# Kernel tuning notes

Measured on AMD Instinct MI355X. Metric: run time of the kernel, lower is better.

## Reference

```python
import jax, jax.numpy as jnp
import numpy as np

B, S, D = 4, 2048, 768
H = 12
DH = D // H
FF = 4 * D
EPS = 1e-5


def _layernorm(x, g, b):
    mu = jnp.mean(x, axis=-1, keepdims=True)
    var = jnp.mean(jnp.square(x - mu), axis=-1, keepdims=True)
    return (x - mu) * jax.lax.rsqrt(var + EPS) * g + b


def setup_inputs() -> dict:
    key = jax.random.key(0)
    ks = jax.random.split(key, 16)
    s_d = 1.0 / np.sqrt(D)
    s_ff = 1.0 / np.sqrt(FF)
    inp = {
        "x": jax.random.normal(ks[0], (B, S, D), jnp.float32),
        # LayerNorm 1
        "ln1_g": jnp.ones((D,), jnp.float32),
        "ln1_b": jnp.zeros((D,), jnp.float32),
        # attention linears (stored as [in, out], i.e. already transposed)
        "Wq": jax.random.normal(ks[1], (D, D), jnp.float32) * s_d,
        "bq": jax.random.normal(ks[2], (D,), jnp.float32) * s_d,
        "Wk": jax.random.normal(ks[3], (D, D), jnp.float32) * s_d,
        "bk": jax.random.normal(ks[4], (D,), jnp.float32) * s_d,
        "Wv": jax.random.normal(ks[5], (D, D), jnp.float32) * s_d,
        "bv": jax.random.normal(ks[6], (D,), jnp.float32) * s_d,
        "Wo": jax.random.normal(ks[7], (D, D), jnp.float32) * s_d,
        "bo": jax.random.normal(ks[8], (D,), jnp.float32) * s_d,
        # LayerNorm 2
        "ln2_g": jnp.ones((D,), jnp.float32),
        "ln2_b": jnp.zeros((D,), jnp.float32),
        # feed-forward (bias always on, per torch code)
        "W1": jax.random.normal(ks[9], (D, FF), jnp.float32) * s_d,
        "b1": jax.random.normal(ks[10], (FF,), jnp.float32) * s_d,
        "W2": jax.random.normal(ks[11], (FF, D), jnp.float32) * s_ff,
        "b2": jax.random.normal(ks[12], (D,), jnp.float32) * s_ff,
    }
    return inp


def reference(x, ln1_g, ln1_b, Wq, bq, Wk, bk, Wv, bv, Wo, bo,
              ln2_g, ln2_b, W1, b1, W2, b2):
    # --- attention branch (pre-LN) ---
    h = _layernorm(x, ln1_g, ln1_b)
    q = (h @ Wq + bq).reshape(B, S, H, DH).transpose(0, 2, 1, 3)  # [B,H,S,DH]
    k = (h @ Wk + bk).reshape(B, S, H, DH).transpose(0, 2, 1, 3)
    v = (h @ Wv + bv).reshape(B, S, H, DH).transpose(0, 2, 1, 3)
    scores = jnp.einsum("bhqd,bhkd->bhqk", q, k) / np.sqrt(DH)
    causal = jnp.tril(jnp.ones((S, S), bool))
    scores = jnp.where(causal, scores, -jnp.inf)
    attn = jax.nn.softmax(scores, axis=-1)
    out = jnp.einsum("bhqk,bhkd->bhqd", attn, v)
    out = out.transpose(0, 2, 1, 3).reshape(B, S, D)
    x = x + (out @ Wo + bo)
    # --- feed-forward branch (pre-LN, exact GELU) ---
    h2 = _layernorm(x, ln2_g, ln2_b)
    ff = jax.nn.gelu(h2 @ W1 + b1, approximate=False) @ W2 + b2
    return x + ff
```

## Files before the change

### kernel.cpp

```cpp
#include <hip/hip_runtime.h>
#include <math.h>

#define B_ 4
#define S_ 2048
#define D_ 768
#define H_ 12
#define DH_ 64
#define FF_ 3072
#define LDQ (3*D_)

using short8  = __attribute__((ext_vector_type(8))) short;
using f32x4   = __attribute__((ext_vector_type(4))) float;
using f32x16  = __attribute__((ext_vector_type(16))) float;
using float4v = __attribute__((ext_vector_type(4))) float;
using ushort4v= __attribute__((ext_vector_type(4))) unsigned short;

__device__ __forceinline__ unsigned short f2bf(float f) {
  unsigned u = __builtin_bit_cast(unsigned, f);
  u += 0x7FFFu + ((u >> 16) & 1u);
  return (unsigned short)(u >> 16);
}

__device__ __forceinline__ unsigned cvt_pk_bf16(float a, float b) {
  unsigned r;
  asm("v_cvt_pk_bf16_f32 %0, %1, %2" : "=v"(r) : "v"(a), "v"(b));
  return r;
}

__device__ __forceinline__ void gload16(const void* g, void* l) {
  __builtin_amdgcn_global_load_lds(
      (const __attribute__((address_space(1))) unsigned*)g,
      (__attribute__((address_space(3))) unsigned*)l, 16, 0, 0);
}

__global__ __launch_bounds__(256) void transpose_cast_multi_kernel(
    const float* __restrict__ Wq, const float* __restrict__ Wk,
    const float* __restrict__ Wv, const float* __restrict__ Wo,
    const float* __restrict__ W1, const float* __restrict__ W2,
    unsigned short* __restrict__ WqT, unsigned short* __restrict__ WkT,
    unsigned short* __restrict__ WvT, unsigned short* __restrict__ WoT,
    unsigned short* __restrict__ W1T, unsigned short* __restrict__ W2T) {
  __shared__ float tile[32][33];
  int bid = blockIdx.x;
  const float* in; unsigned short* out; int K, N, t;
  if (bid < 2304) {
    int seg = bid / 576; t = bid % 576; K = D_; N = D_;
    in  = seg == 0 ? Wq  : seg == 1 ? Wk  : seg == 2 ? Wv  : Wo;
    out = seg == 0 ? WqT : seg == 1 ? WkT : seg == 2 ? WvT : WoT;
  } else if (bid < 4608) {
    t = bid - 2304; K = D_; N = FF_; in = W1; out = W1T;
  } else {
    t = bid - 4608; K = FF_; N = D_; in = W2; out = W2T;
  }
  int ntk = K / 32;
  int k0 = (t % ntk) * 32, n0 = (t / ntk) * 32;
  int tx = threadIdx.x, ty = threadIdx.y;
#pragma unroll
  for (int i = 0; i < 4; i++)
    tile[ty + 8*i][tx] = in[(size_t)(k0 + ty + 8*i) * N + n0 + tx];
  __syncthreads();
#pragma unroll
  for (int i = 0; i < 4; i++)
    out[(size_t)(n0 + ty + 8*i) * K + k0 + tx] = f2bf(tile[tx][ty + 8*i]);
}

__global__ void bias_cat_kernel(const float* __restrict__ bq, const float* __restrict__ bk,
                                const float* __restrict__ bv, float* __restrict__ dst) {
  int i = blockIdx.x * 256 + threadIdx.x;
  if (i >= 3 * D_) return;
  float v;
  if (i < D_)            v = bq[i];
  else if (i < 2 * D_)   v = bk[i - D_];
  else                   v = bv[i - 2 * D_];
  dst[i] = v;
}

__global__ __launch_bounds__(256) void layernorm_kernel(
    const float* __restrict__ x, const float* __restrict__ g,
    const float* __restrict__ b, unsigned short* __restrict__ out) {
  int wave = threadIdx.x >> 6, lane = threadIdx.x & 63;
  int row = blockIdx.x * 4 + wave;
  const float* xr = x + (size_t)row * D_;
  float4v v[3];
  float sum = 0.f, sq = 0.f;
#pragma unroll
  for (int i = 0; i < 3; i++) {
    v[i] = reinterpret_cast<const float4v*>(xr)[lane + 64*i];
#pragma unroll
    for (int j = 0; j < 4; j++) { sum += v[i][j]; sq += v[i][j]*v[i][j]; }
  }
#pragma unroll
  for (int d = 1; d < 64; d <<= 1) { sum += __shfl_xor(sum, d); sq += __shfl_xor(sq, d); }
  float mu   = sum * (1.0f / D_);
  float var  = sq  * (1.0f / D_) - mu * mu;
  float rstd = rsqrtf(var + 1e-5f);
  unsigned short* orow = out + (size_t)row * D_;
#pragma unroll
  for (int i = 0; i < 3; i++) {
    int idx = (lane + 64*i) * 4;
    ushort4v o;
#pragma unroll
    for (int j = 0; j < 4; j++)
      o[j] = f2bf((v[i][j] - mu) * rstd * g[idx + j] + b[idx + j]);
    *reinterpret_cast<ushort4v*>(orow + idx) = o;
  }
}

#define EPI_QKV   0
#define EPI_OPROJ 1
#define EPI_GELU  2
#define EPI_FINAL 3

template<int EPI>
__global__ __launch_bounds__(256) void gemm_kernel(
    const unsigned short* __restrict__ A, int lda,
    const unsigned short* __restrict__ BT, int K,
    const float* __restrict__ bias,
    const float* __restrict__ resid,
    float* __restrict__ outf,
    unsigned short* __restrict__ outh,
    int ldo, float ascale, int nN) {
  __shared__ __attribute__((aligned(16))) unsigned short Ls[3][128*64];
  int tid = threadIdx.x;
  int wave = tid >> 6, lane = tid & 63;
  int lrow = lane & 15, lk = lane >> 4;
  int bid = blockIdx.x;
  int xcd = bid & 7, j = bid >> 3;
  int nM8 = gridDim.x / (8 * nN);
  int m0 = (xcd * nM8 + j / nN) * 128;
  int n0 = (j % nN) * 128;
  int wm = (wave >> 1) * 64, wn = (wave & 1) * 64;

  auto STAGE = [&](int buf, int k0) {
#pragma unroll
    for (int i = 0; i < 4; i++) {
      int ch = i * 256 + tid;
      int row = ch >> 3, s8 = ch & 7;
      int m = s8 ^ (row & 7);
      const unsigned short* src = (m < 4)
        ? A  + (size_t)(m0 + row) * lda + k0 + m * 8
        : BT + (size_t)(n0 + row) * K   + k0 + (m - 4) * 8;
      gload16(src, &Ls[buf][(i*256 + wave*64) * 8]);
    }
  };

  f32x4 acc[4][4] = {};
  int nt = K / 32;
  STAGE(0, 0);
  STAGE(1, 32);
  for (int t = 0; t < nt; t++) {
    if (t + 1 < nt) { asm volatile("s_waitcnt vmcnt(4)" ::: "memory"); }
    else            { asm volatile("s_waitcnt vmcnt(0)" ::: "memory"); }
    __builtin_amdgcn_s_barrier();
    const unsigned short* Lc = Ls[t % 3];
    short8 af[4], bf[4];
#pragma unroll
    for (int mi = 0; mi < 4; mi++) {
      int row = wm + mi*16 + lrow;
      af[mi] = *reinterpret_cast<const short8*>(&Lc[row*64 + ((lk ^ (row & 7)) * 8)]);
    }
#pragma unroll
    for (int ni = 0; ni < 4; ni++) {
      int row = wn + ni*16 + lrow;
      bf[ni] = *reinterpret_cast<const short8*>(&Lc[row*64 + (((4 + lk) ^ (row & 7)) * 8)]);
    }
    if (t + 2 < nt) STAGE((t + 2) % 3, (t + 2) * 32);
    __builtin_amdgcn_s_setprio(1);
#pragma unroll
    for (int mi = 0; mi < 4; mi++)
#pragma unroll
      for (int ni = 0; ni < 4; ni++)
        acc[mi][ni] = __builtin_amdgcn_mfma_f32_16x16x32_bf16(af[mi], bf[ni], acc[mi][ni], 0, 0, 0);
    __builtin_amdgcn_s_setprio(0);
  }
#pragma unroll
  for (int mi = 0; mi < 4; mi++) {
#pragma unroll
    for (int ni = 0; ni < 4; ni++) {
#pragma unroll
      for (int r = 0; r < 4; r++) {
        int gm = m0 + wm + mi*16 + (lane >> 4)*4 + r;
        int gn = n0 + wn + ni*16 + lrow;
        float v = acc[mi][ni][r] + bias[gn];
        if constexpr (EPI == EPI_QKV) {
          if (gn < D_) v *= ascale;
          outh[(size_t)gm * ldo + gn] = f2bf(v);
        } else if constexpr (EPI == EPI_OPROJ) {
          size_t idx = (size_t)gm * ldo + gn;
          outf[idx] = v + resid[idx];
        } else if constexpr (EPI == EPI_GELU) {
          float gv = 0.5f * v * (1.0f + erff(v * 0.70710678118654752f));
          outh[(size_t)gm * ldo + gn] = f2bf(gv);
        } else {
          size_t idx = (size_t)gm * ldo + gn;
          outf[idx] = v + resid[idx];
        }
      }
    }
  }
}

__global__ __launch_bounds__(256) void attn_kernel(
    const unsigned short* __restrict__ qkv,
    unsigned short* __restrict__ o) {
  __shared__ __attribute__((aligned(16))) unsigned short Ks[2][64*64];
  __shared__ __attribute__((aligned(16))) unsigned short VT[2][64*64];
  __shared__ __attribute__((aligned(16))) unsigned short P2[4][32*64];
  int tid = threadIdx.x;
  int wave = tid >> 6, lane = tid & 63;
  int ql = lane & 31, hi = lane >> 5;
  int bid = blockIdx.x;
  int xcd = bid & 7, r = bid >> 3;
  int bh = xcd * 6 + (r % 6);
  int qtile = 15 - (r / 6);
  int bb = bh / H_, hh = bh % H_;
  const unsigned short* qb = qkv + (size_t)bb * S_ * LDQ + hh * DH_;
  const unsigned short* kb = qb + D_;
  const unsigned short* vb = qb + 2 * D_;
  unsigned short* Pw = P2[wave];
  int swq = (ql & 7) << 4;

  int sr = tid >> 2;
  int sc16 = (tid & 3) * 16;
  int kp = tid & 31, dh0 = (tid >> 5) * 8;
  uint4 krA, krB, vrA, vrB;

  auto LOADR = [&](int kb0) {
    const unsigned short* ksrc = kb + (size_t)(kb0 + sr) * LDQ + sc16;
    krA = *reinterpret_cast<const uint4*>(ksrc);
    krB = *reinterpret_cast<const uint4*>(ksrc + 8);
    const unsigned short* vsrc = vb + (size_t)(kb0 + 2*kp) * LDQ + dh0;
    vrA = *reinterpret_cast<const uint4*>(vsrc);
    vrB = *reinterpret_cast<const uint4*>(vsrc + LDQ);
  };
  auto WRITE = [&](int buf) {
    int sw = (sr & 7) << 4;
    int cb = sc16 * 2;
    *reinterpret_cast<uint4*>(&Ks[buf][(sr*128 + (cb ^ sw)) >> 1]) = krA;
    *reinterpret_cast<uint4*>(&Ks[buf][(sr*128 + ((cb + 16) ^ sw)) >> 1]) = krB;
    union { uint4 u4; unsigned short s[8]; } a, b;
    a.u4 = vrA; b.u4 = vrB;
#pragma unroll
    for (int j2 = 0; j2 < 8; j2++) {
      int row = dh0 + j2, sw2 = (row & 7) << 4;
      *reinterpret_cast<unsigned*>(&VT[buf][(row*128 + ((4*kp) ^ sw2)) >> 1]) =
          (unsigned)a.s[j2] | ((unsigned)b.s[j2] << 16);
    }
  };

  int q0 = qtile * 128;
  int qw = q0 + wave * 32;
  int myq = qw + ql;

  short8 qf[4];
#pragma unroll
  for (int dblk = 0; dblk < 4; dblk++)
    qf[dblk] = *reinterpret_cast<const short8*>(qb + (size_t)myq * LDQ + dblk*16 + hi*8);

  f32x16 oaccT[2] = {};
  float mst = -1e30f, lst = 0.f;
  int nt = q0 / 64 + 2;

  LOADR(0);
  WRITE(0);
  __syncthreads();

  for (int kt = 0; kt < nt; kt++) {
    int kb0 = kt * 64;
    int cur = kt & 1;
    if (kt + 1 < nt) LOADR((kt + 1) * 64);

    if (kb0 <= qw + 31) {
      f32x16 sc[2] = {};
      __builtin_amdgcn_s_setprio(1);
#pragma unroll
      for (int dblk = 0; dblk < 4; dblk++) {
#pragma unroll
        for (int blk = 0; blk < 2; blk++) {
          int row = blk*32 + ql;
          int sw = (row & 7) << 4;
          short8 kf = *reinterpret_cast<const short8*>(
              &Ks[cur][(row*128 + (((unsigned)(dblk*32 + hi*16)) ^ sw)) >> 1]);
          sc[blk] = __builtin_amdgcn_mfma_f32_32x32x16_bf16(kf, qf[dblk], sc[blk], 0, 0, 0);
        }
      }
      __builtin_amdgcn_s_setprio(0);
      bool full = (kb0 + 63 <= qw);
      if (!full) {
#pragma unroll
        for (int blk = 0; blk < 2; blk++)
#pragma unroll
          for (int r2 = 0; r2 < 16; r2++) {
            int key = kb0 + blk*32 + (r2 & 3) + 8*(r2 >> 2) + 4*hi;
            if (key > myq) sc[blk][r2] = -1e30f;
          }
      }
      float pm0 = -1e30f, pm1 = -1e30f, pm2 = -1e30f, pm3 = -1e30f;
#pragma unroll
      for (int blk = 0; blk < 2; blk++)
#pragma unroll
        for (int g = 0; g < 4; g++) {
          pm0 = fmaxf(pm0, sc[blk][4*g]);
          pm1 = fmaxf(pm1, sc[blk][4*g+1]);
          pm2 = fmaxf(pm2, sc[blk][4*g+2]);
          pm3 = fmaxf(pm3, sc[blk][4*g+3]);
        }
      float mx = fmaxf(fmaxf(pm0, pm1), fmaxf(pm2, pm3));
      mx = fmaxf(mx, __shfl_xor(mx, 32));
      if (!__all(mx <= mst + 8.0f)) {
        float mnew = fmaxf(mst, mx);
        float fac = exp2f(mst - mnew);
        lst *= fac;
#pragma unroll
        for (int db = 0; db < 2; db++)
#pragma unroll
          for (int r2 = 0; r2 < 16; r2++) oaccT[db][r2] *= fac;
        mst = mnew;
      }
      float ps0 = 0.f, ps1 = 0.f, ps2 = 0.f, ps3 = 0.f;
#pragma unroll
      for (int blk = 0; blk < 2; blk++)
#pragma unroll
        for (int g = 0; g < 4; g++) {
          float p0 = exp2f(sc[blk][4*g]   - mst);
          float p1 = exp2f(sc[blk][4*g+1] - mst);
          float p2 = exp2f(sc[blk][4*g+2] - mst);
          float p3 = exp2f(sc[blk][4*g+3] - mst);
          ps0 += p0; ps1 += p1; ps2 += p2; ps3 += p3;
          uint2 val;
          val.x = cvt_pk_bf16(p0, p1);
          val.y = cvt_pk_bf16(p2, p3);
          int cbyte = (blk*64 + g*16 + hi*8) ^ swq;
          *reinterpret_cast<uint2*>(&Pw[(ql*128 + cbyte) >> 1]) = val;
        }
      float rs = (ps0 + ps1) + (ps2 + ps3);
      rs += __shfl_xor(rs, 32);
      lst += rs;
      __builtin_amdgcn_s_setprio(1);
#pragma unroll
      for (int ks = 0; ks < 4; ks++) {
        int cb = ks*32 + hi*16;
        short8 pa = *reinterpret_cast<const short8*>(&Pw[(ql*128 + (cb ^ swq)) >> 1]);
#pragma unroll
        for (int db = 0; db < 2; db++) {
          int row = db*32 + ql;
          int sw = (row & 7) << 4;
          short8 vf = *reinterpret_cast<const short8*>(&VT[cur][(row*128 + (cb ^ sw)) >> 1]);
          oaccT[db] = __builtin_amdgcn_mfma_f32_32x32x16_bf16(vf, pa, oaccT[db], 0, 0, 0);
        }
      }
      __builtin_amdgcn_s_setprio(0);
    }

    if (kt + 1 < nt) WRITE((kt + 1) & 1);
    __syncthreads();
  }

  float inv = 1.0f / lst;
  unsigned short* ob = o + ((size_t)(bb * S_ + myq)) * D_ + hh * DH_;
#pragma unroll
  for (int db = 0; db < 2; db++)
#pragma unroll
    for (int g = 0; g < 8; g++) {
      int r2 = 2 * g;
      int dh = db*32 + (r2 & 3) + 8*(r2 >> 2) + 4*hi;
      unsigned pk = cvt_pk_bf16(oaccT[db][r2] * inv, oaccT[db][r2+1] * inv);
      *reinterpret_cast<unsigned*>(ob + dh) = pk;
    }
}

extern "C" void kernel_launch(void* const* d_in, const int* in_sizes, int n_in,
                              void* d_out, int out_size, void* d_ws, size_t ws_size,
                              hipStream_t stream) {
  (void)in_sizes; (void)n_in; (void)out_size; (void)ws_size;
  const float* x    = (const float*)d_in[0];
  const float* ln1g = (const float*)d_in[1];
  const float* ln1b = (const float*)d_in[2];
  const float* Wq   = (const float*)d_in[3];
  const float* bq   = (const float*)d_in[4];
  const float* Wk   = (const float*)d_in[5];
  const float* bk   = (const float*)d_in[6];
  const float* Wv   = (const float*)d_in[7];
  const float* bv   = (const float*)d_in[8];
  const float* Wo   = (const float*)d_in[9];
  const float* bo   = (const float*)d_in[10];
  const float* ln2g = (const float*)d_in[11];
  const float* ln2b = (const float*)d_in[12];
  const float* W1   = (const float*)d_in[13];
  const float* b1   = (const float*)d_in[14];
  const float* W2   = (const float*)d_in[15];
  const float* b2   = (const float*)d_in[16];
  float* out = (float*)d_out;

  char* ws = (char*)d_ws;
  size_t off = 0;
  auto alloc = [&](size_t bytes) {
    char* p = ws + off;
    off += (bytes + 255) & ~(size_t)255;
    return p;
  };
  unsigned short* WqT = (unsigned short*)alloc((size_t)D_*D_*2);
  unsigned short* WkT = (unsigned short*)alloc((size_t)D_*D_*2);
  unsigned short* WvT = (unsigned short*)alloc((size_t)D_*D_*2);
  unsigned short* WoT = (unsigned short*)alloc((size_t)D_*D_*2);
  unsigned short* W1T = (unsigned short*)alloc((size_t)D_*FF_*2);
  unsigned short* W2T = (unsigned short*)alloc((size_t)FF_*D_*2);
  unsigned short* h   = (unsigned short*)alloc((size_t)B_*S_*D_*2);
  unsigned short* qkv = (unsigned short*)alloc((size_t)B_*S_*LDQ*2);
  unsigned short* ob  = (unsigned short*)alloc((size_t)B_*S_*D_*2);
  float* bias_cat     = (float*)alloc((size_t)3*D_*4);
  unsigned short* ffb = qkv;
  unsigned short* h2  = h;

  const float qscale = 0.125f * 1.4426950408889634f;

  dim3 tb(32, 8);
  transpose_cast_multi_kernel<<<6912, tb, 0, stream>>>(
      Wq, Wk, Wv, Wo, W1, W2, WqT, WkT, WvT, WoT, W1T, W2T);
  bias_cat_kernel<<<9, 256, 0, stream>>>(bq, bk, bv, bias_cat);

  layernorm_kernel<<<(B_*S_)/4, 256, 0, stream>>>(x, ln1g, ln1b, h);

  gemm_kernel<EPI_QKV><<<dim3(64*18), 256, 0, stream>>>(
      h, D_, WqT, D_, bias_cat, nullptr, nullptr, qkv, LDQ, qscale, 18);

  attn_kernel<<<dim3(768), 256, 0, stream>>>(qkv, ob);

  gemm_kernel<EPI_OPROJ><<<dim3(64*6), 256, 0, stream>>>(
      ob, D_, WoT, D_, bo, x, out, nullptr, D_, 1.0f, 6);

  layernorm_kernel<<<(B_*S_)/4, 256, 0, stream>>>(out, ln2g, ln2b, h2);

  gemm_kernel<EPI_GELU><<<dim3(64*24), 256, 0, stream>>>(
      h2, D_, W1T, D_, b1, nullptr, nullptr, ffb, FF_, 1.0f, 24);

  gemm_kernel<EPI_FINAL><<<dim3(64*6), 256, 0, stream>>>(
      ffb, FF_, W2T, FF_, b2, out, out, nullptr, D_, 1.0f, 6);
}
```

Before: 278.3 us.

## Split causal attention across key ranges with a pairing and a merge kernel

The attention kernel now pairs query tile p with tile 15-p. Each block processes the first part of one tile's key range and the second part of the other's, so every block runs the same number of key tiles instead of between 2 and 32. Each pass writes unnormalized bf16 partial outputs plus its running max and sum to a workspace buffer. A new merge kernel rescales and combines the two partials per query row and writes the normalized output. This trades the causal load imbalance for an extra kernel launch, extra global traffic for the partials, and a small bf16 rounding step on the intermediate results.

```diff
diff --git a/kernel.cpp b/kernel.cpp
--- a/kernel.cpp
+++ b/kernel.cpp
@@ -19,6 +19,11 @@
   unsigned u = __builtin_bit_cast(unsigned, f);
   u += 0x7FFFu + ((u >> 16) & 1u);
   return (unsigned short)(u >> 16);
+}
+
+__device__ __forceinline__ float bf2f(unsigned short h) {
+  unsigned u = ((unsigned)h) << 16;
+  return __builtin_bit_cast(float, u);
 }
 
 __device__ __forceinline__ unsigned cvt_pk_bf16(float a, float b) {
@@ -200,9 +205,9 @@
   }
 }
 
-__global__ __launch_bounds__(256) void attn_kernel(
+__global__ __launch_bounds__(256) void attn_partial_kernel(
     const unsigned short* __restrict__ qkv,
-    unsigned short* __restrict__ o) {
+    unsigned short* __restrict__ part) {
   __shared__ __attribute__((aligned(16))) unsigned short Ks[2][64*64];
   __shared__ __attribute__((aligned(16))) unsigned short VT[2][64*64];
   __shared__ __attribute__((aligned(16))) unsigned short P2[4][32*64];
@@ -212,7 +217,7 @@
   int bid = blockIdx.x;
   int xcd = bid & 7, r = bid >> 3;
   int bh = xcd * 6 + (r % 6);
-  int qtile = 15 - (r / 6);
+  int p = r / 6;
   int bb = bh / H_, hh = bh % H_;
   const unsigned short* qb = qkv + (size_t)bb * S_ * LDQ + hh * DH_;
   const unsigned short* kb = qb + D_;
@@ -248,125 +253,181 @@
     }
   };
 
-  int q0 = qtile * 128;
-  int qw = q0 + wave * 32;
-  int myq = qw + ql;
-
-  short8 qf[4];
-#pragma unroll
-  for (int dblk = 0; dblk < 4; dblk++)
-    qf[dblk] = *reinterpret_cast<const short8*>(qb + (size_t)myq * LDQ + dblk*16 + hi*8);
-
-  f32x16 oaccT[2] = {};
-  float mst = -1e30f, lst = 0.f;
-  int nt = q0 / 64 + 2;
-
-  LOADR(0);
-  WRITE(0);
-  __syncthreads();
-
-  for (int kt = 0; kt < nt; kt++) {
-    int kb0 = kt * 64;
-    int cur = kt & 1;
-    if (kt + 1 < nt) LOADR((kt + 1) * 64);
-
-    if (kb0 <= qw + 31) {
-      f32x16 sc[2] = {};
-      __builtin_amdgcn_s_setprio(1);
-#pragma unroll
-      for (int dblk = 0; dblk < 4; dblk++) {
-#pragma unroll
-        for (int blk = 0; blk < 2; blk++) {
-          int row = blk*32 + ql;
-          int sw = (row & 7) << 4;
-          short8 kf = *reinterpret_cast<const short8*>(
-              &Ks[cur][(row*128 + (((unsigned)(dblk*32 + hi*16)) ^ sw)) >> 1]);
-          sc[blk] = __builtin_amdgcn_mfma_f32_32x32x16_bf16(kf, qf[dblk], sc[blk], 0, 0, 0);
+#pragma unroll 1
+  for (int pass = 0; pass < 2; pass++) {
+    int qtile = pass == 0 ? p : (15 - p);
+    int kt0   = pass == 0 ? 0 : (16 - p);
+    int kt1   = pass == 0 ? (p + 1) : (32 - 2 * p);
+    int q0 = qtile * 128;
+    int qw = q0 + wave * 32;
+    int myq = qw + ql;
+
+    short8 qf[4];
+#pragma unroll
+    for (int dblk = 0; dblk < 4; dblk++)
+      qf[dblk] = *reinterpret_cast<const short8*>(qb + (size_t)myq * LDQ + dblk*16 + hi*8);
+
+    f32x16 oaccT[2] = {};
+    float mst = -1e30f, lst = 0.f;
+
+    LOADR(kt0 * 64);
+    WRITE(0);
+    __syncthreads();
+
+    for (int kt = kt0; kt < kt1; kt++) {
+      int kb0 = kt * 64;
+      int cur = (kt - kt0) & 1;
+      if (kt + 1 < kt1) LOADR((kt + 1) * 64);
+
+      if (kb0 <= qw + 31) {
+        f32x16 sc[2] = {};
+        __builtin_amdgcn_s_setprio(1);
+#pragma unroll
+        for (int dblk = 0; dblk < 4; dblk++) {
+#pragma unroll
+          for (int blk = 0; blk < 2; blk++) {
+            int row = blk*32 + ql;
+            int sw = (row & 7) << 4;
+            short8 kf = *reinterpret_cast<const short8*>(
+                &Ks[cur][(row*128 + (((unsigned)(dblk*32 + hi*16)) ^ sw)) >> 1]);
+            sc[blk] = __builtin_amdgcn_mfma_f32_32x32x16_bf16(kf, qf[dblk], sc[blk], 0, 0, 0);
+          }
         }
+        __builtin_amdgcn_s_setprio(0);
+        bool full = (kb0 + 63 <= qw);
+        if (!full) {
+#pragma unroll
+          for (int blk = 0; blk < 2; blk++)
+#pragma unroll
+            for (int r2 = 0; r2 < 16; r2++) {
+              int key = kb0 + blk*32 + (r2 & 3) + 8*(r2 >> 2) + 4*hi;
+              if (key > myq) sc[blk][r2] = -1e30f;
+            }
+        }
+        float pm0 = -1e30f, pm1 = -1e30f, pm2 = -1e30f, pm3 = -1e30f;
+#pragma unroll
+        for (int blk = 0; blk < 2; blk++)
+#pragma unroll
+          for (int g = 0; g < 4; g++) {
+            pm0 = fmaxf(pm0, sc[blk][4*g]);
+            pm1 = fmaxf(pm1, sc[blk][4*g+1]);
+            pm2 = fmaxf(pm2, sc[blk][4*g+2]);
+            pm3 = fmaxf(pm3, sc[blk][4*g+3]);
+          }
+        float mx = fmaxf(fmaxf(pm0, pm1), fmaxf(pm2, pm3));
+        mx = fmaxf(mx, __shfl_xor(mx, 32));
+        if (!__all(mx <= mst + 8.0f)) {
+          float mnew = fmaxf(mst, mx);
+          float fac = exp2f(mst - mnew);
+          lst *= fac;
+#pragma unroll
+          for (int db = 0; db < 2; db++)
+#pragma unroll
+            for (int r2 = 0; r2 < 16; r2++) oaccT[db][r2] *= fac;
+          mst = mnew;
+        }
+        float ps0 = 0.f, ps1 = 0.f, ps2 = 0.f, ps3 = 0.f;
+#pragma unroll
+        for (int blk = 0; blk < 2; blk++)
+#pragma unroll
+          for (int g = 0; g < 4; g++) {
+            float p0 = exp2f(sc[blk][4*g]   - mst);
+            float p1 = exp2f(sc[blk][4*g+1] - mst);
+            float p2 = exp2f(sc[blk][4*g+2] - mst);
+            float p3 = exp2f(sc[blk][4*g+3] - mst);
+            ps0 += p0; ps1 += p1; ps2 += p2; ps3 += p3;
+            uint2 val;
+            val.x = cvt_pk_bf16(p0, p1);
+            val.y = cvt_pk_bf16(p2, p3);
+            int cbyte = (blk*64 + g*16 + hi*8) ^ swq;
+            *reinterpret_cast<uint2*>(&Pw[(ql*128 + cbyte) >> 1]) = val;
+          }
+        float rs = (ps0 + ps1) + (ps2 + ps3);
+        rs += __shfl_xor(rs, 32);
+        lst += rs;
+        __builtin_amdgcn_s_setprio(1);
+#pragma unroll
+        for (int ks = 0; ks < 4; ks++) {
+          int cb = ks*32 + hi*16;
+          short8 pa = *reinterpret_cast<const short8*>(&Pw[(ql*128 + (cb ^ swq)) >> 1]);
+#pragma unroll
+          for (int db = 0; db < 2; db++) {
+            int row = db*32 + ql;
+            int sw = (row & 7) << 4;
+            short8 vf = *reinterpret_cast<const short8*>(&VT[cur][(row*128 + (cb ^ sw)) >> 1]);
+            oaccT[db] = __builtin_amdgcn_mfma_f32_32x32x16_bf16(vf, pa, oaccT[db], 0, 0, 0);
+          }
+        }
+        __builtin_amdgcn_s_setprio(0);
       }
-      __builtin_amdgcn_s_setprio(0);
-      bool full = (kb0 + 63 <= qw);
-      if (!full) {
-#pragma unroll
-        for (int blk = 0; blk < 2; blk++)
-#pragma unroll
-          for (int r2 = 0; r2 < 16; r2++) {
-            int key = kb0 + blk*32 + (r2 & 3) + 8*(r2 >> 2) + 4*hi;
-            if (key > myq) sc[blk][r2] = -1e30f;
-          }
+
+      if (kt + 1 < kt1) WRITE(((kt + 1 - kt0) & 1));
+      __syncthreads();
+    }
+
+    unsigned short* pp = part + ((size_t)(pass * 48 + bh) * S_ + myq) * 72;
+#pragma unroll
+    for (int db = 0; db < 2; db++)
+#pragma unroll
+      for (int g = 0; g < 4; g++) {
+        int r2 = 4 * g;
+        uint2 val;
+        val.x = cvt_pk_bf16(oaccT[db][r2],     oaccT[db][r2 + 1]);
+        val.y = cvt_pk_bf16(oaccT[db][r2 + 2], oaccT[db][r2 + 3]);
+        int dh = db*32 + 8*g + 4*hi;
+        *reinterpret_cast<uint2*>(pp + dh) = val;
       }
-      float pm0 = -1e30f, pm1 = -1e30f, pm2 = -1e30f, pm3 = -1e30f;
-#pragma unroll
-      for (int blk = 0; blk < 2; blk++)
-#pragma unroll
-        for (int g = 0; g < 4; g++) {
-          pm0 = fmaxf(pm0, sc[blk][4*g]);
-          pm1 = fmaxf(pm1, sc[blk][4*g+1]);
-          pm2 = fmaxf(pm2, sc[blk][4*g+2]);
-          pm3 = fmaxf(pm3, sc[blk][4*g+3]);
-        }
-      float mx = fmaxf(fmaxf(pm0, pm1), fmaxf(pm2, pm3));
-      mx = fmaxf(mx, __shfl_xor(mx, 32));
-      if (!__all(mx <= mst + 8.0f)) {
-        float mnew = fmaxf(mst, mx);
-        float fac = exp2f(mst - mnew);
-        lst *= fac;
-#pragma unroll
-        for (int db = 0; db < 2; db++)
-#pragma unroll
-          for (int r2 = 0; r2 < 16; r2++) oaccT[db][r2] *= fac;
-        mst = mnew;
-      }
-      float ps0 = 0.f, ps1 = 0.f, ps2 = 0.f, ps3 = 0.f;
-#pragma unroll
-      for (int blk = 0; blk < 2; blk++)
-#pragma unroll
-        for (int g = 0; g < 4; g++) {
-          float p0 = exp2f(sc[blk][4*g]   - mst);
-          float p1 = exp2f(sc[blk][4*g+1] - mst);
-          float p2 = exp2f(sc[blk][4*g+2] - mst);
-          float p3 = exp2f(sc[blk][4*g+3] - mst);
-          ps0 += p0; ps1 += p1; ps2 += p2; ps3 += p3;
-          uint2 val;
-          val.x = cvt_pk_bf16(p0, p1);
-          val.y = cvt_pk_bf16(p2, p3);
-          int cbyte = (blk*64 + g*16 + hi*8) ^ swq;
-          *reinterpret_cast<uint2*>(&Pw[(ql*128 + cbyte) >> 1]) = val;
-        }
-      float rs = (ps0 + ps1) + (ps2 + ps3);
-      rs += __shfl_xor(rs, 32);
-      lst += rs;
-      __builtin_amdgcn_s_setprio(1);
-#pragma unroll
-      for (int ks = 0; ks < 4; ks++) {
-        int cb = ks*32 + hi*16;
-        short8 pa = *reinterpret_cast<const short8*>(&Pw[(ql*128 + (cb ^ swq)) >> 1]);
-#pragma unroll
-        for (int db = 0; db < 2; db++) {
-          int row = db*32 + ql;
-          int sw = (row & 7) << 4;
-          short8 vf = *reinterpret_cast<const short8*>(&VT[cur][(row*128 + (cb ^ sw)) >> 1]);
-          oaccT[db] = __builtin_amdgcn_mfma_f32_32x32x16_bf16(vf, pa, oaccT[db], 0, 0, 0);
-        }
-      }
-      __builtin_amdgcn_s_setprio(0);
-    }
-
-    if (kt + 1 < nt) WRITE((kt + 1) & 1);
-    __syncthreads();
-  }
-
-  float inv = 1.0f / lst;
-  unsigned short* ob = o + ((size_t)(bb * S_ + myq)) * D_ + hh * DH_;
-#pragma unroll
-  for (int db = 0; db < 2; db++)
-#pragma unroll
-    for (int g = 0; g < 8; g++) {
-      int r2 = 2 * g;
-      int dh = db*32 + (r2 & 3) + 8*(r2 >> 2) + 4*hi;
-      unsigned pk = cvt_pk_bf16(oaccT[db][r2] * inv, oaccT[db][r2+1] * inv);
-      *reinterpret_cast<unsigned*>(ob + dh) = pk;
-    }
+    if (hi == 0) {
+      float2 ml; ml.x = mst; ml.y = lst;
+      *reinterpret_cast<float2*>(pp + 64) = ml;
+    }
+  }
+}
+
+__global__ __launch_bounds__(256) void attn_merge_kernel(
+    const unsigned short* __restrict__ part,
+    unsigned short* __restrict__ o) {
+  int bid = blockIdx.x;
+  int xcd = bid & 7, r = bid >> 3;
+  int bh = xcd * 6 + (r % 6);
+  int rowblk = r / 6;
+  int tid = threadIdx.x;
+  int rl = tid >> 2, q4 = tid & 3;
+  int qrow = rowblk * 64 + rl;
+  int bb = bh / H_, hh = bh % H_;
+  const unsigned short* pa = part + ((size_t)bh * S_ + qrow) * 72;
+  const unsigned short* pb = pa + (size_t)48 * S_ * 72;
+  float2 mla = *reinterpret_cast<const float2*>(pa + 64);
+  float2 mlb = *reinterpret_cast<const float2*>(pb + 64);
+  float m = fmaxf(mla.x, mlb.x);
+  float wa = exp2f(mla.x - m), wb = exp2f(mlb.x - m);
+  float inv = 1.0f / (mla.y * wa + mlb.y * wb);
+  float fa = wa * inv, fb = wb * inv;
+  const uint4* va = reinterpret_cast<const uint4*>(pa + q4 * 16);
+  const uint4* vb = reinterpret_cast<const uint4*>(pb + q4 * 16);
+  uint4 a0 = va[0], a1 = va[1], b0 = vb[0], b1 = vb[1];
+  unsigned short* op = o + ((size_t)(bb * S_ + qrow)) * D_ + hh * DH_ + q4 * 16;
+  uint4 o0, o1;
+  unsigned* ao = reinterpret_cast<unsigned*>(&a0);
+  unsigned* bo = reinterpret_cast<unsigned*>(&b0);
+  unsigned* oo = reinterpret_cast<unsigned*>(&o0);
+#pragma unroll
+  for (int i = 0; i < 4; i++) {
+    float lo = fa * bf2f((unsigned short)(ao[i] & 0xFFFF)) + fb * bf2f((unsigned short)(bo[i] & 0xFFFF));
+    float hi2 = fa * bf2f((unsigned short)(ao[i] >> 16))   + fb * bf2f((unsigned short)(bo[i] >> 16));
+    oo[i] = cvt_pk_bf16(lo, hi2);
+  }
+  ao = reinterpret_cast<unsigned*>(&a1);
+  bo = reinterpret_cast<unsigned*>(&b1);
+  oo = reinterpret_cast<unsigned*>(&o1);
+#pragma unroll
+  for (int i = 0; i < 4; i++) {
+    float lo = fa * bf2f((unsigned short)(ao[i] & 0xFFFF)) + fb * bf2f((unsigned short)(bo[i] & 0xFFFF));
+    float hi2 = fa * bf2f((unsigned short)(ao[i] >> 16))   + fb * bf2f((unsigned short)(bo[i] >> 16));
+    oo[i] = cvt_pk_bf16(lo, hi2);
+  }
+  reinterpret_cast<uint4*>(op)[0] = o0;
+  reinterpret_cast<uint4*>(op)[1] = o1;
 }
 
 extern "C" void kernel_launch(void* const* d_in, const int* in_sizes, int n_in,
@@ -409,6 +470,7 @@
   unsigned short* qkv = (unsigned short*)alloc((size_t)B_*S_*LDQ*2);
   unsigned short* ob  = (unsigned short*)alloc((size_t)B_*S_*D_*2);
   float* bias_cat     = (float*)alloc((size_t)3*D_*4);
+  unsigned short* part= (unsigned short*)alloc((size_t)2*48*S_*72*2);
   unsigned short* ffb = qkv;
   unsigned short* h2  = h;
 
@@ -424,7 +486,8 @@
   gemm_kernel<EPI_QKV><<<dim3(64*18), 256, 0, stream>>>(
       h, D_, WqT, D_, bias_cat, nullptr, nullptr, qkv, LDQ, qscale, 18);
 
-  attn_kernel<<<dim3(768), 256, 0, stream>>>(qkv, ob);
+  attn_partial_kernel<<<dim3(768), 256, 0, stream>>>(qkv, part);
+  attn_merge_kernel<<<dim3(1536), 256, 0, stream>>>(part, ob);
 
   gemm_kernel<EPI_OPROJ><<<dim3(64*6), 256, 0, stream>>>(
       ob, D_, WoT, D_, bo, x, out, nullptr, D_, 1.0f, 6);
```

Measured after the change: 291.6 us. 1.05x slower.

## Keep attention probabilities in registers via permlane32 swap instead of LDS round-trip

Applied to the files above, without the earlier changes.

The P matrix is no longer written to and read back from per-wave shared memory. The MFMA output fragments are converted to bf16 and rearranged in registers with v_permlane32_swap, so they form the A-operand layout directly. This drops 16KB of LDS and the store/load latency. The loop is also unrolled by two with constant buffer indices, and launch bounds now request 3 waves per SIMD, which risks register pressure. nt is always even here (q0/64 is even), so the two-step loop stays correct.

```diff
diff --git a/kernel.cpp b/kernel.cpp
--- a/kernel.cpp
+++ b/kernel.cpp
@@ -200,12 +200,11 @@
   }
 }
 
-__global__ __launch_bounds__(256) void attn_kernel(
+__global__ __launch_bounds__(256, 3) void attn_kernel(
     const unsigned short* __restrict__ qkv,
     unsigned short* __restrict__ o) {
   __shared__ __attribute__((aligned(16))) unsigned short Ks[2][64*64];
   __shared__ __attribute__((aligned(16))) unsigned short VT[2][64*64];
-  __shared__ __attribute__((aligned(16))) unsigned short P2[4][32*64];
   int tid = threadIdx.x;
   int wave = tid >> 6, lane = tid & 63;
   int ql = lane & 31, hi = lane >> 5;
@@ -217,8 +216,6 @@
   const unsigned short* qb = qkv + (size_t)bb * S_ * LDQ + hh * DH_;
   const unsigned short* kb = qb + D_;
   const unsigned short* vb = qb + 2 * D_;
-  unsigned short* Pw = P2[wave];
-  int swq = (ql & 7) << 4;
 
   int sr = tid >> 2;
   int sc16 = (tid & 3) * 16;
@@ -261,14 +258,10 @@
   float mst = -1e30f, lst = 0.f;
   int nt = q0 / 64 + 2;
 
-  LOADR(0);
-  WRITE(0);
-  __syncthreads();
-
-  for (int kt = 0; kt < nt; kt++) {
+  auto TILE = [&](int kt, int cur) {
     int kb0 = kt * 64;
-    int cur = kt & 1;
-    if (kt + 1 < nt) LOADR((kt + 1) * 64);
+    bool has_next = (kt + 1 < nt);
+    if (has_next) LOADR((kt + 1) * 64);
 
     if (kb0 <= qw + 31) {
       f32x16 sc[2] = {};
@@ -317,43 +310,59 @@
           for (int r2 = 0; r2 < 16; r2++) oaccT[db][r2] *= fac;
         mst = mnew;
       }
-      float ps0 = 0.f, ps1 = 0.f, ps2 = 0.f, ps3 = 0.f;
-#pragma unroll
-      for (int blk = 0; blk < 2; blk++)
-#pragma unroll
-        for (int g = 0; g < 4; g++) {
-          float p0 = exp2f(sc[blk][4*g]   - mst);
-          float p1 = exp2f(sc[blk][4*g+1] - mst);
-          float p2 = exp2f(sc[blk][4*g+2] - mst);
-          float p3 = exp2f(sc[blk][4*g+3] - mst);
-          ps0 += p0; ps1 += p1; ps2 += p2; ps3 += p3;
-          uint2 val;
-          val.x = cvt_pk_bf16(p0, p1);
-          val.y = cvt_pk_bf16(p2, p3);
-          int cbyte = (blk*64 + g*16 + hi*8) ^ swq;
-          *reinterpret_cast<uint2*>(&Pw[(ql*128 + cbyte) >> 1]) = val;
+      short8 pa[4];
+      float rs = 0.f;
+#pragma unroll
+      for (int b = 0; b < 2; b++) {
+#pragma unroll
+        for (int so = 0; so < 2; so++) {
+          float p0 = exp2f(sc[b][8*so + 0] - mst);
+          float p1 = exp2f(sc[b][8*so + 1] - mst);
+          float p2 = exp2f(sc[b][8*so + 2] - mst);
+          float p3 = exp2f(sc[b][8*so + 3] - mst);
+          float p4 = exp2f(sc[b][8*so + 4] - mst);
+          float p5 = exp2f(sc[b][8*so + 5] - mst);
+          float p6 = exp2f(sc[b][8*so + 6] - mst);
+          float p7 = exp2f(sc[b][8*so + 7] - mst);
+          rs += ((p0 + p1) + (p2 + p3)) + ((p4 + p5) + (p6 + p7));
+          unsigned W0 = cvt_pk_bf16(p0, p1);
+          unsigned W1 = cvt_pk_bf16(p2, p3);
+          unsigned W2 = cvt_pk_bf16(p4, p5);
+          unsigned W3 = cvt_pk_bf16(p6, p7);
+          asm volatile("v_permlane32_swap_b32 %0, %1" : "+v"(W0), "+v"(W2));
+          asm volatile("v_permlane32_swap_b32 %0, %1" : "+v"(W1), "+v"(W3));
+          union { uint4 u; short8 s; } cvtu;
+          cvtu.u.x = W0; cvtu.u.y = W1; cvtu.u.z = W2; cvtu.u.w = W3;
+          pa[2*b + so] = cvtu.s;
         }
-      float rs = (ps0 + ps1) + (ps2 + ps3);
+      }
       rs += __shfl_xor(rs, 32);
       lst += rs;
       __builtin_amdgcn_s_setprio(1);
 #pragma unroll
       for (int ks = 0; ks < 4; ks++) {
         int cb = ks*32 + hi*16;
-        short8 pa = *reinterpret_cast<const short8*>(&Pw[(ql*128 + (cb ^ swq)) >> 1]);
 #pragma unroll
         for (int db = 0; db < 2; db++) {
           int row = db*32 + ql;
           int sw = (row & 7) << 4;
           short8 vf = *reinterpret_cast<const short8*>(&VT[cur][(row*128 + (cb ^ sw)) >> 1]);
-          oaccT[db] = __builtin_amdgcn_mfma_f32_32x32x16_bf16(vf, pa, oaccT[db], 0, 0, 0);
+          oaccT[db] = __builtin_amdgcn_mfma_f32_32x32x16_bf16(vf, pa[ks], oaccT[db], 0, 0, 0);
         }
       }
       __builtin_amdgcn_s_setprio(0);
     }
 
-    if (kt + 1 < nt) WRITE((kt + 1) & 1);
+    if (has_next) WRITE(cur ^ 1);
     __syncthreads();
+  };
+
+  LOADR(0);
+  WRITE(0);
+  __syncthreads();
+  for (int kt = 0; kt < nt; kt += 2) {
+    TILE(kt, 0);
+    TILE(kt + 1, 1);
   }
 
   float inv = 1.0f / lst;
```

Result: faster. 264.3 us (-5.0%).
